# Kernel tuning notes

Hardware: AMD Instinct MI355X
Metric: run time of the kernel (lower is better)

The kernel has to match this reference:

```python
import jax, jax.numpy as jnp
import numpy as np

B, S, D = 4, 2048, 2048
NH, NKV = 16, 4
HD = D // NH  # 128


def setup_inputs() -> dict:
    key = jax.random.key(0)
    ks = jax.random.split(key, 6)
    sd = 1.0 / np.sqrt(D)
    return {
        "x": jax.random.normal(ks[0], (B, S, D), jnp.float32),
        "cos": jax.random.normal(ks[1], (1, 1, S, HD), jnp.float32),
        "sin": jax.random.normal(ks[2], (1, 1, S, HD), jnp.float32),
        "wq_w": jax.random.normal(ks[3], (D, D), jnp.float32) * sd,
        "wk_w": jax.random.normal(ks[4], (NKV * HD, D), jnp.float32) * sd,
        "wv_w": jax.random.normal(ks[5], (NKV * HD, D), jnp.float32) * sd,
        "start_pos": 0,
    }


def _rotate_half(t):
    h = t.shape[-1] // 2
    return jnp.concatenate([-t[..., h:], t[..., :h]], axis=-1)


def reference(x, cos, sin, wq_w, wk_w, wv_w, start_pos):
    b, s, d = x.shape
    n_rep = NH // NKV
    q = (x @ wq_w.T).reshape(b, s, NH, HD).transpose(0, 2, 1, 3)      # [b,H,s,hd]
    k = (x @ wk_w.T).reshape(b, s, NKV, HD).transpose(0, 2, 1, 3)     # [b,Hk,s,hd]
    v = (x @ wv_w.T).reshape(b, s, NKV, HD).transpose(0, 2, 1, 3)
    # rotary
    q = q * cos + _rotate_half(q) * sin
    k = k * cos + _rotate_half(k) * sin
    # repeat_kv
    k = jnp.repeat(k, n_rep, axis=1)   # [b,H,s,hd]
    v = jnp.repeat(v, n_rep, axis=1)
    scores = jnp.einsum("bhqd,bhkd->bhqk", q, k) / jnp.sqrt(jnp.float32(HD))
    causal = jnp.tril(jnp.ones((s, s), dtype=bool))
    scores = jnp.where(causal, scores, jnp.float32(-jnp.inf))
    w = jax.nn.softmax(scores, axis=-1)
    out = jnp.einsum("bhqk,bhkd->bhqd", w, v)
    return out.transpose(0, 2, 1, 3).reshape(b, s, d)
```

## Files before the change

kernel.cpp:

```cpp
#include <hip/hip_runtime.h>
#include <hip/hip_bf16.h>
#include <math.h>

#define B_ 4
#define S_ 2048
#define D_ 2048
#define NH_ 16
#define NKV_ 4
#define HD_ 128

typedef short bf16x8 __attribute__((ext_vector_type(8)));
typedef float f32x4 __attribute__((ext_vector_type(4)));
typedef __hip_bfloat16 bf16;

#define ASYNC_CP16(gp, lp)                                                    \
  __builtin_amdgcn_global_load_lds(                                           \
      (const __attribute__((address_space(1))) unsigned int*)(gp),            \
      (__attribute__((address_space(3))) unsigned int*)(lp), 16, 0, 0)

__global__ __launch_bounds__(256) void cvt_kernel(const float* __restrict__ in,
                                                  bf16* __restrict__ out, int n4) {
  int i = blockIdx.x * 256 + threadIdx.x;
  if (i >= n4) return;
  float4 v = ((const float4*)in)[i];
  union { ushort4 u; bf16 h[4]; } o;
  o.h[0] = __float2bfloat16(v.x);
  o.h[1] = __float2bfloat16(v.y);
  o.h[2] = __float2bfloat16(v.z);
  o.h[3] = __float2bfloat16(v.w);
  ((ushort4*)out)[i] = o.u;
}

__global__ __launch_bounds__(256) void gemm_qkv(
    const bf16* __restrict__ A, const bf16* __restrict__ W,
    bf16* __restrict__ qr, bf16* __restrict__ kr, bf16* __restrict__ vlin,
    const float* __restrict__ cosp, const float* __restrict__ sinp,
    float qscale) {
  __shared__ __align__(16) bf16 As[128 * 64];
  __shared__ __align__(16) bf16 Bs[128 * 64];
  const int tid = threadIdx.x;
  const int lane = tid & 63, wave = tid >> 6;
  const int m0 = blockIdx.x * 128;
  const int hblk = blockIdx.y;
  const int n0 = hblk * 128;
  const int quad = lane >> 4, c = lane & 15;
  const int K = 2048;

  f32x4 acc[2][8] = {};

  const int sr = lane >> 3;
  const int sg = lane & 7;
  const int gc = (sg ^ sr) * 8;
  const bf16* Ap = A + (size_t)(m0 + wave * 32 + sr) * K + gc;
  const bf16* Bp = W + (size_t)(n0 + wave * 32 + sr) * K + gc;

  for (int kb = 0; kb < K; kb += 64) {
    __syncthreads();
#pragma unroll
    for (int i = 0; i < 4; i++) {
      ASYNC_CP16(Ap + (size_t)(i * 8) * K + kb, &As[(wave * 32 + i * 8) * 64]);
      ASYNC_CP16(Bp + (size_t)(i * 8) * K + kb, &Bs[(wave * 32 + i * 8) * 64]);
    }
    __syncthreads();
#pragma unroll
    for (int kk = 0; kk < 2; kk++) {
      const int slot = ((kk * 4 + quad) ^ (c & 7)) * 8;
      bf16x8 af[2], bfr[8];
#pragma unroll
      for (int t = 0; t < 2; t++)
        af[t] = *(const bf16x8*)(&As[(wave * 32 + t * 16 + c) * 64 + slot]);
#pragma unroll
      for (int t = 0; t < 8; t++)
        bfr[t] = *(const bf16x8*)(&Bs[(t * 16 + c) * 64 + slot]);
#pragma unroll
      for (int mt = 0; mt < 2; mt++)
#pragma unroll
        for (int nt = 0; nt < 8; nt++)
          acc[mt][nt] = __builtin_amdgcn_mfma_f32_16x16x32_bf16(
              af[mt], bfr[nt], acc[mt][nt], 0, 0, 0);
    }
  }

  if (hblk < 20) {
    const float scale = (hblk < 16) ? qscale : 1.0f;
#pragma unroll
    for (int mt = 0; mt < 2; mt++)
#pragma unroll
      for (int reg = 0; reg < 4; reg++) {
        int m = m0 + wave * 32 + mt * 16 + quad * 4 + reg;
        int b = m >> 11, s = m & 2047;
        const float* cr = cosp + s * HD_;
        const float* sn = sinp + s * HD_;
        bf16* orow = (hblk < 16)
            ? qr + ((size_t)(b * NH_ + hblk) * S_ + s) * HD_
            : kr + ((size_t)(b * NKV_ + (hblk - 16)) * S_ + s) * HD_;
#pragma unroll
        for (int nt = 0; nt < 4; nt++) {
          int d1 = nt * 16 + c, d2 = d1 + 64;
          float q1 = acc[mt][nt][reg], q2 = acc[mt][nt + 4][reg];
          float o1 = (q1 * cr[d1] - q2 * sn[d1]) * scale;
          float o2 = (q2 * cr[d2] + q1 * sn[d2]) * scale;
          orow[d1] = __float2bfloat16(o1);
          orow[d2] = __float2bfloat16(o2);
        }
      }
  } else {
    bf16* vbase = vlin + (size_t)(hblk - 20) * HD_;
#pragma unroll
    for (int mt = 0; mt < 2; mt++)
#pragma unroll
      for (int reg = 0; reg < 4; reg++) {
        int m = m0 + wave * 32 + mt * 16 + quad * 4 + reg;
        bf16* row = vbase + (size_t)m * (NKV_ * HD_);
#pragma unroll
        for (int nt = 0; nt < 8; nt++)
          row[nt * 16 + c] = __float2bfloat16(acc[mt][nt][reg]);
      }
  }
}

__global__ __launch_bounds__(256) void v_transpose(const bf16* __restrict__ in,
                                                   int instride,
                                                   bf16* __restrict__ out) {
  __shared__ __align__(16) bf16 tile[64][HD_ + 8];
  int bidx = blockIdx.x;
  int st = bidx & 31;
  int kv = (bidx >> 5) & 3;
  int b = bidx >> 7;
  int s0 = st * 64;
  int t = threadIdx.x;
  {
    int row = t >> 2;
    int colb = (t & 3) * 32;
#pragma unroll
    for (int i = 0; i < 4; i++) {
      int col = colb + i * 8;
      *(uint4*)(&tile[row][col]) = *(const uint4*)(
          &in[(size_t)(b * S_ + s0 + row) * instride + kv * HD_ + col]);
    }
  }
  __syncthreads();
  int sl = t & 63, hb = t >> 6;
#pragma unroll
  for (int i = 0; i < 32; i++) {
    int hd = i * 4 + hb;
    out[((size_t)(b * NKV_ + kv) * HD_ + hd) * S_ + s0 + sl] = tile[sl][hd];
  }
}

__device__ __forceinline__ void attn_step(
    const bf16* __restrict__ Ks, const bf16* __restrict__ Vs,
    bf16* __restrict__ Psw, const bf16x8* qf, f32x4* o,
    float& m_i, float& l_i, bool diag, int kb, int qbase, int quad, int c) {
  f32x4 sacc[4] = {};
#pragma unroll
  for (int kt = 0; kt < 4; kt++) {
    const int slot = ((kt * 4 + quad) ^ (c & 7)) * 8;
#pragma unroll
    for (int mt = 0; mt < 4; mt++) {
      bf16x8 kf = *(const bf16x8*)(&Ks[(mt * 16 + c) * 128 + slot]);
      sacc[mt] = __builtin_amdgcn_mfma_f32_16x16x32_bf16(kf, qf[kt], sacc[mt], 0, 0, 0);
    }
  }
  if (diag) {
    const int qg = qbase + c;
#pragma unroll
    for (int mt = 0; mt < 4; mt++)
#pragma unroll
      for (int r = 0; r < 4; r++)
        if (kb + mt * 16 + quad * 4 + r > qg) sacc[mt][r] = -INFINITY;
  }
  float mx = sacc[0][0];
#pragma unroll
  for (int mt = 0; mt < 4; mt++)
#pragma unroll
    for (int r = 0; r < 4; r++) mx = fmaxf(mx, sacc[mt][r]);
  mx = fmaxf(mx, __shfl_xor(mx, 16, 64));
  mx = fmaxf(mx, __shfl_xor(mx, 32, 64));
  const float mnew = fmaxf(m_i, mx);
  const float alpha = exp2f(m_i - mnew);
  m_i = mnew;
  float rs = 0.f;
#pragma unroll
  for (int mt = 0; mt < 4; mt++) {
    float p0 = exp2f(sacc[mt][0] - mnew);
    float p1 = exp2f(sacc[mt][1] - mnew);
    float p2 = exp2f(sacc[mt][2] - mnew);
    float p3 = exp2f(sacc[mt][3] - mnew);
    rs += (p0 + p1) + (p2 + p3);
    unsigned u0 = __builtin_bit_cast(unsigned, p0) + 0x8000u;
    unsigned u1 = __builtin_bit_cast(unsigned, p1) + 0x8000u;
    unsigned u2 = __builtin_bit_cast(unsigned, p2) + 0x8000u;
    unsigned u3 = __builtin_bit_cast(unsigned, p3) + 0x8000u;
    uint2 pk;
    pk.x = __builtin_amdgcn_perm(u1, u0, 0x07060302u);
    pk.y = __builtin_amdgcn_perm(u3, u2, 0x07060302u);
    *(uint2*)(&Psw[c * 72 + mt * 16 + quad * 4]) = pk;
  }
  rs += __shfl_xor(rs, 16, 64);
  rs += __shfl_xor(rs, 32, 64);
  l_i = l_i * alpha + rs;
  if (__any(alpha != 1.0f)) {
    float a0 = __shfl(alpha, quad * 4 + 0, 64);
    float a1 = __shfl(alpha, quad * 4 + 1, 64);
    float a2 = __shfl(alpha, quad * 4 + 2, 64);
    float a3 = __shfl(alpha, quad * 4 + 3, 64);
#pragma unroll
    for (int nt = 0; nt < 8; nt++) {
      o[nt][0] *= a0; o[nt][1] *= a1; o[nt][2] *= a2; o[nt][3] *= a3;
    }
  }
#pragma unroll
  for (int kk = 0; kk < 2; kk++) {
    bf16x8 pf = *(const bf16x8*)(&Psw[c * 72 + kk * 32 + quad * 8]);
    const int slot = ((kk * 4 + quad) ^ (c & 7)) * 8;
#pragma unroll
    for (int nt = 0; nt < 8; nt++) {
      bf16x8 vf = *(const bf16x8*)(&Vs[(nt * 16 + c) * 64 + slot]);
      o[nt] = __builtin_amdgcn_mfma_f32_16x16x32_bf16(pf, vf, o[nt], 0, 0, 0);
    }
  }
}

__global__ __launch_bounds__(256) void attn_kernel(const bf16* __restrict__ Q,
                                                   const bf16* __restrict__ Kr,
                                                   const bf16* __restrict__ Vt,
                                                   float* __restrict__ O) {
  __shared__ __align__(16) bf16 Ks[64 * 128];
  __shared__ __align__(16) bf16 Vs[128 * 64];
  __shared__ __align__(16) bf16 Ps[4][16 * 72];

  const int tid = threadIdx.x, lane = tid & 63, wave = tid >> 6;
  const int quad = lane >> 4, c = lane & 15;
  const int j = blockIdx.x;
  const int bh = blockIdx.y;
  const int b = bh >> 4, h = bh & 15, kv = h >> 2;
  bf16* Psw = &Ps[wave][0];

  const bf16* kbase = Kr + (size_t)(b * NKV_ + kv) * S_ * HD_;
  const bf16* vbase = Vt + (size_t)(b * NKV_ + kv) * HD_ * S_;

  int koff[4], voff;
  {
    const int kl = lane >> 4;
    const int ks = lane & 15;
#pragma unroll
    for (int i = 0; i < 4; i++) {
      int r = wave * 16 + i * 4 + kl;
      koff[i] = r * HD_ + ((ks ^ (r & 7)) * 8);
    }
    const int vl = lane >> 3;
    const int vs = lane & 7;
    voff = (wave * 32 + vl) * S_ + ((vs ^ (vl & 7)) * 8);
  }

#pragma unroll 1
  for (int pass = 0; pass < 2; ++pass) {
    const int qt = pass ? (31 - j) : j;
    const int q0 = qt * 64;
    const int qb = q0 + wave * 16;

    bf16x8 qf[4];
    {
      const bf16* qp = Q + ((size_t)(b * NH_ + h) * S_ + qb + c) * HD_;
#pragma unroll
      for (int kt = 0; kt < 4; kt++)
        qf[kt] = *(const bf16x8*)(qp + kt * 32 + quad * 8);
    }
    f32x4 o_acc[8] = {};
    float m_i = -INFINITY, l_i = 0.f;

#pragma unroll 1
    for (int it = 0; it <= qt; ++it) {
      const int kb = it * 64;
      __syncthreads();
#pragma unroll
      for (int i = 0; i < 4; i++) {
        ASYNC_CP16(kbase + (size_t)kb * HD_ + koff[i], &Ks[(wave * 16 + i * 4) * 128]);
        ASYNC_CP16(vbase + kb + voff + (size_t)(i * 8) * S_, &Vs[(wave * 32 + i * 8) * 64]);
      }
      __syncthreads();
      attn_step(Ks, Vs, Psw, qf, o_acc, m_i, l_i, it == qt, kb, qb, quad, c);
    }

    float inv[4];
#pragma unroll
    for (int r = 0; r < 4; r++) inv[r] = 1.0f / __shfl(l_i, quad * 4 + r, 64);
    float* obase = O + (size_t)b * S_ * D_ + (size_t)h * HD_;
#pragma unroll
    for (int nt = 0; nt < 8; nt++)
#pragma unroll
      for (int r = 0; r < 4; r++)
        obase[(size_t)(qb + quad * 4 + r) * D_ + nt * 16 + c] = o_acc[nt][r] * inv[r];
  }
}

extern "C" void kernel_launch(void* const* d_in, const int* in_sizes, int n_in,
                              void* d_out, int out_size, void* d_ws, size_t ws_size,
                              hipStream_t stream) {
  const float* x    = (const float*)d_in[0];
  const float* cosp = (const float*)d_in[1];
  const float* sinp = (const float*)d_in[2];
  const float* wq   = (const float*)d_in[3];
  const float* wk   = (const float*)d_in[4];
  const float* wv   = (const float*)d_in[5];
  float* out = (float*)d_out;

  char* ws = (char*)d_ws;
  const size_t MB = 1024 * 1024;
  bf16* xb    = (bf16*)(ws + 0);
  bf16* wqkvb = (bf16*)(ws + 32 * MB);
  bf16* qr    = (bf16*)(ws + 44 * MB);
  bf16* kr    = (bf16*)(ws + 76 * MB);
  bf16* vlin  = (bf16*)(ws + 84 * MB);
  bf16* vt    = (bf16*)(ws + 92 * MB);

  cvt_kernel<<<16384, 256, 0, stream>>>(x, xb, 4194304);
  cvt_kernel<<<4096, 256, 0, stream>>>(wq, wqkvb, 1048576);
  cvt_kernel<<<1024, 256, 0, stream>>>(wk, wqkvb + 4194304, 262144);
  cvt_kernel<<<1024, 256, 0, stream>>>(wv, wqkvb + 5242880, 262144);

  const float qscale = 1.4426950408889634f / 11.313708498984761f;
  gemm_qkv<<<dim3(64, 24), 256, 0, stream>>>(xb, wqkvb, qr, kr, vlin,
                                             cosp, sinp, qscale);

  v_transpose<<<512, 256, 0, stream>>>(vlin, NKV_ * HD_, vt);

  attn_kernel<<<dim3(16, 64), 256, 0, stream>>>(qr, kr, vt, out);
}
```

Measured before the change: 426.2 us.

## Use 2x2 wave tiling in QKV GEMM and vectorize attention softmax with swizzled P

The QKV projection GEMM changes from each wave owning 32 rows by all 128 columns to a 2x2 wave grid of 64x64 tiles, which cuts per-wave LDS fragment loads. The rotary epilogue now exchanges the second half of each head through shared memory, so only two waves write Q/K outputs. The attention softmax is rewritten with vector max, exp and scale operations, the P tile uses an XOR-swizzled layout without padding, and the attention kernel gets a min-blocks occupancy hint of 4. The risks are an extra sync and LDS round trip in the GEMM epilogue, half the waves sitting idle during the rotary write, and register pressure from the occupancy bound.

```diff
diff --git a/kernel.cpp b/kernel.cpp
--- a/kernel.cpp
+++ b/kernel.cpp
@@ -11,6 +11,7 @@
 
 typedef short bf16x8 __attribute__((ext_vector_type(8)));
 typedef float f32x4 __attribute__((ext_vector_type(4)));
+typedef unsigned u32x4 __attribute__((ext_vector_type(4)));
 typedef __hip_bfloat16 bf16;
 
 #define ASYNC_CP16(gp, lp)                                                    \
@@ -40,13 +41,14 @@
   __shared__ __align__(16) bf16 Bs[128 * 64];
   const int tid = threadIdx.x;
   const int lane = tid & 63, wave = tid >> 6;
+  const int wm = (wave & 1) * 64, wn = (wave >> 1) * 64;
   const int m0 = blockIdx.x * 128;
   const int hblk = blockIdx.y;
   const int n0 = hblk * 128;
   const int quad = lane >> 4, c = lane & 15;
   const int K = 2048;
 
-  f32x4 acc[2][8] = {};
+  f32x4 acc[4][4] = {};
 
   const int sr = lane >> 3;
   const int sg = lane & 7;
@@ -65,57 +67,74 @@
 #pragma unroll
     for (int kk = 0; kk < 2; kk++) {
       const int slot = ((kk * 4 + quad) ^ (c & 7)) * 8;
-      bf16x8 af[2], bfr[8];
-#pragma unroll
-      for (int t = 0; t < 2; t++)
-        af[t] = *(const bf16x8*)(&As[(wave * 32 + t * 16 + c) * 64 + slot]);
-#pragma unroll
-      for (int t = 0; t < 8; t++)
-        bfr[t] = *(const bf16x8*)(&Bs[(t * 16 + c) * 64 + slot]);
-#pragma unroll
-      for (int mt = 0; mt < 2; mt++)
-#pragma unroll
-        for (int nt = 0; nt < 8; nt++)
+      bf16x8 af[4], bfr[4];
+#pragma unroll
+      for (int t = 0; t < 4; t++) {
+        af[t]  = *(const bf16x8*)(&As[(wm + t * 16 + c) * 64 + slot]);
+        bfr[t] = *(const bf16x8*)(&Bs[(wn + t * 16 + c) * 64 + slot]);
+      }
+#pragma unroll
+      for (int mt = 0; mt < 4; mt++)
+#pragma unroll
+        for (int nt = 0; nt < 4; nt++)
           acc[mt][nt] = __builtin_amdgcn_mfma_f32_16x16x32_bf16(
               af[mt], bfr[nt], acc[mt][nt], 0, 0, 0);
     }
   }
 
-  if (hblk < 20) {
-    const float scale = (hblk < 16) ? qscale : 1.0f;
-#pragma unroll
-    for (int mt = 0; mt < 2; mt++)
+  if (hblk >= 20) {
+    const int colb = (hblk - 20) * 128 + wn;
+#pragma unroll
+    for (int mt = 0; mt < 4; mt++)
 #pragma unroll
       for (int reg = 0; reg < 4; reg++) {
-        int m = m0 + wave * 32 + mt * 16 + quad * 4 + reg;
-        int b = m >> 11, s = m & 2047;
-        const float* cr = cosp + s * HD_;
-        const float* sn = sinp + s * HD_;
-        bf16* orow = (hblk < 16)
-            ? qr + ((size_t)(b * NH_ + hblk) * S_ + s) * HD_
-            : kr + ((size_t)(b * NKV_ + (hblk - 16)) * S_ + s) * HD_;
-#pragma unroll
-        for (int nt = 0; nt < 4; nt++) {
-          int d1 = nt * 16 + c, d2 = d1 + 64;
-          float q1 = acc[mt][nt][reg], q2 = acc[mt][nt + 4][reg];
-          float o1 = (q1 * cr[d1] - q2 * sn[d1]) * scale;
-          float o2 = (q2 * cr[d2] + q1 * sn[d2]) * scale;
-          orow[d1] = __float2bfloat16(o1);
-          orow[d2] = __float2bfloat16(o2);
-        }
+        int m = m0 + wm + mt * 16 + quad * 4 + reg;
+        bf16* row = vlin + (size_t)m * (NKV_ * HD_) + colb;
+#pragma unroll
+        for (int nt = 0; nt < 4; nt++)
+          row[nt * 16 + c] = __float2bfloat16(acc[mt][nt][reg]);
       }
   } else {
-    bf16* vbase = vlin + (size_t)(hblk - 20) * HD_;
-#pragma unroll
-    for (int mt = 0; mt < 2; mt++)
-#pragma unroll
-      for (int reg = 0; reg < 4; reg++) {
-        int m = m0 + wave * 32 + mt * 16 + quad * 4 + reg;
-        bf16* row = vbase + (size_t)m * (NKV_ * HD_);
-#pragma unroll
-        for (int nt = 0; nt < 8; nt++)
-          row[nt * 16 + c] = __float2bfloat16(acc[mt][nt][reg]);
-      }
+    float* Sc = (float*)As;
+    __syncthreads();
+    if (wave >= 2) {
+#pragma unroll
+      for (int mt = 0; mt < 4; mt++)
+#pragma unroll
+        for (int reg = 0; reg < 4; reg++) {
+          int lr = wm + mt * 16 + quad * 4 + reg;
+#pragma unroll
+          for (int nt = 0; nt < 4; nt++)
+            Sc[lr * 64 + nt * 16 + c] = acc[mt][nt][reg];
+        }
+    }
+    __syncthreads();
+    if (wave < 2) {
+      const float scale = (hblk < 16) ? qscale : 1.0f;
+#pragma unroll
+      for (int mt = 0; mt < 4; mt++)
+#pragma unroll
+        for (int reg = 0; reg < 4; reg++) {
+          int lr = wm + mt * 16 + quad * 4 + reg;
+          int m = m0 + lr;
+          int b = m >> 11, s = m & 2047;
+          const float* cr = cosp + s * HD_;
+          const float* sn = sinp + s * HD_;
+          bf16* orow = (hblk < 16)
+              ? qr + ((size_t)(b * NH_ + hblk) * S_ + s) * HD_
+              : kr + ((size_t)(b * NKV_ + (hblk - 16)) * S_ + s) * HD_;
+#pragma unroll
+          for (int nt = 0; nt < 4; nt++) {
+            int d1 = nt * 16 + c, d2 = d1 + 64;
+            float q1 = acc[mt][nt][reg];
+            float q2 = Sc[lr * 64 + d1];
+            float o1 = (q1 * cr[d1] - q2 * sn[d1]) * scale;
+            float o2 = (q2 * cr[d2] + q1 * sn[d2]) * scale;
+            orow[d1] = __float2bfloat16(o1);
+            orow[d2] = __float2bfloat16(o2);
+          }
+        }
+    }
   }
 }
 
@@ -170,49 +189,47 @@
       for (int r = 0; r < 4; r++)
         if (kb + mt * 16 + quad * 4 + r > qg) sacc[mt][r] = -INFINITY;
   }
-  float mx = sacc[0][0];
-#pragma unroll
-  for (int mt = 0; mt < 4; mt++)
-#pragma unroll
-    for (int r = 0; r < 4; r++) mx = fmaxf(mx, sacc[mt][r]);
+  f32x4 mx4 = __builtin_elementwise_max(
+      __builtin_elementwise_max(sacc[0], sacc[1]),
+      __builtin_elementwise_max(sacc[2], sacc[3]));
+  float mx = fmaxf(fmaxf(mx4[0], mx4[1]), fmaxf(mx4[2], mx4[3]));
   mx = fmaxf(mx, __shfl_xor(mx, 16, 64));
   mx = fmaxf(mx, __shfl_xor(mx, 32, 64));
   const float mnew = fmaxf(m_i, mx);
   const float alpha = exp2f(m_i - mnew);
   m_i = mnew;
-  float rs = 0.f;
+  const f32x4 mn4 = {mnew, mnew, mnew, mnew};
+  f32x4 rs4 = {0.f, 0.f, 0.f, 0.f};
 #pragma unroll
   for (int mt = 0; mt < 4; mt++) {
-    float p0 = exp2f(sacc[mt][0] - mnew);
-    float p1 = exp2f(sacc[mt][1] - mnew);
-    float p2 = exp2f(sacc[mt][2] - mnew);
-    float p3 = exp2f(sacc[mt][3] - mnew);
-    rs += (p0 + p1) + (p2 + p3);
-    unsigned u0 = __builtin_bit_cast(unsigned, p0) + 0x8000u;
-    unsigned u1 = __builtin_bit_cast(unsigned, p1) + 0x8000u;
-    unsigned u2 = __builtin_bit_cast(unsigned, p2) + 0x8000u;
-    unsigned u3 = __builtin_bit_cast(unsigned, p3) + 0x8000u;
+    f32x4 e = sacc[mt] - mn4;
+    f32x4 p;
+    p[0] = exp2f(e[0]); p[1] = exp2f(e[1]);
+    p[2] = exp2f(e[2]); p[3] = exp2f(e[3]);
+    rs4 += p;
+    u32x4 u = __builtin_bit_cast(u32x4, p) + 0x8000u;
     uint2 pk;
-    pk.x = __builtin_amdgcn_perm(u1, u0, 0x07060302u);
-    pk.y = __builtin_amdgcn_perm(u3, u2, 0x07060302u);
-    *(uint2*)(&Psw[c * 72 + mt * 16 + quad * 4]) = pk;
-  }
+    pk.x = __builtin_amdgcn_perm(u[1], u[0], 0x07060302u);
+    pk.y = __builtin_amdgcn_perm(u[3], u[2], 0x07060302u);
+    const int pslot = mt * 2 + (quad >> 1);
+    *(uint2*)(&Psw[c * 64 + ((pslot ^ (c & 7)) << 3) + (quad & 1) * 4]) = pk;
+  }
+  float rs = (rs4[0] + rs4[1]) + (rs4[2] + rs4[3]);
   rs += __shfl_xor(rs, 16, 64);
   rs += __shfl_xor(rs, 32, 64);
   l_i = l_i * alpha + rs;
   if (__any(alpha != 1.0f)) {
-    float a0 = __shfl(alpha, quad * 4 + 0, 64);
-    float a1 = __shfl(alpha, quad * 4 + 1, 64);
-    float a2 = __shfl(alpha, quad * 4 + 2, 64);
-    float a3 = __shfl(alpha, quad * 4 + 3, 64);
-#pragma unroll
-    for (int nt = 0; nt < 8; nt++) {
-      o[nt][0] *= a0; o[nt][1] *= a1; o[nt][2] *= a2; o[nt][3] *= a3;
-    }
+    f32x4 av;
+    av[0] = __shfl(alpha, quad * 4 + 0, 64);
+    av[1] = __shfl(alpha, quad * 4 + 1, 64);
+    av[2] = __shfl(alpha, quad * 4 + 2, 64);
+    av[3] = __shfl(alpha, quad * 4 + 3, 64);
+#pragma unroll
+    for (int nt = 0; nt < 8; nt++) o[nt] *= av;
   }
 #pragma unroll
   for (int kk = 0; kk < 2; kk++) {
-    bf16x8 pf = *(const bf16x8*)(&Psw[c * 72 + kk * 32 + quad * 8]);
+    bf16x8 pf = *(const bf16x8*)(&Psw[c * 64 + (((kk * 4 + quad) ^ (c & 7)) << 3)]);
     const int slot = ((kk * 4 + quad) ^ (c & 7)) * 8;
 #pragma unroll
     for (int nt = 0; nt < 8; nt++) {
@@ -222,13 +239,13 @@
   }
 }
 
-__global__ __launch_bounds__(256) void attn_kernel(const bf16* __restrict__ Q,
-                                                   const bf16* __restrict__ Kr,
-                                                   const bf16* __restrict__ Vt,
-                                                   float* __restrict__ O) {
+__global__ __launch_bounds__(256, 4) void attn_kernel(const bf16* __restrict__ Q,
+                                                      const bf16* __restrict__ Kr,
+                                                      const bf16* __restrict__ Vt,
+                                                      float* __restrict__ O) {
   __shared__ __align__(16) bf16 Ks[64 * 128];
   __shared__ __align__(16) bf16 Vs[128 * 64];
-  __shared__ __align__(16) bf16 Ps[4][16 * 72];
+  __shared__ __align__(16) bf16 Ps[4][16 * 64];
 
   const int tid = threadIdx.x, lane = tid & 63, wave = tid >> 6;
   const int quad = lane >> 4, c = lane & 15;
```

Result: faster. 388.1 us (-9.0%).
